# Kernel tuning notes

Hardware: AMD Instinct MI355X
Metric: run time of the kernel (lower is better)

The kernel has to match this reference:

```python
import jax, jax.numpy as jnp
import numpy as np

H = 64  # lstm_units
FORGET_BIAS = 1.0  # TF LSTMCell default


def setup_inputs() -> dict:
    key = jax.random.key(0)
    k1, k2, k3 = jax.random.split(key, 3)
    B, T = 256, 2048
    x = jax.random.normal(k1, (B, T, 1), dtype=jnp.float32)
    # Layer 1: LSTMCell(64), input dim 1 -> kernel [(1+64), 4*64]
    W1 = jax.random.normal(k2, (1 + H, 4 * H), dtype=jnp.float32) * 0.1
    b1 = jnp.zeros((4 * H,), dtype=jnp.float32)
    # Layer 2: LSTMCell(1), input dim 64 -> kernel [(64+1), 4*1]
    W2 = jax.random.normal(k3, (H + 1, 4), dtype=jnp.float32) * 0.1
    b2 = jnp.zeros((4,), dtype=jnp.float32)
    return {"x": x, "W1": W1, "b1": b1, "W2": W2, "b2": b2}


def _lstm_step(c, h, xt, W, b):
    # TF LSTMCell: gates from concat([x, h]) @ W + b, order i, j, f, o
    z = jnp.concatenate([xt, h], axis=-1) @ W + b
    i, j, f, o = jnp.split(z, 4, axis=-1)
    c_new = jax.nn.sigmoid(f + FORGET_BIAS) * c + jax.nn.sigmoid(i) * jnp.tanh(j)
    h_new = jax.nn.sigmoid(o) * jnpp_tanh(c_new) if False else jax.nn.sigmoid(o) * jnp.tanh(c_new)
    return c_new, h_new


def reference(x, W1, b1, W2, b2):
    # x: [B, T, 1] -> outputs of 2-layer stacked LSTM, final layer size 1
    B = x.shape[0]

    def step(carry, xt):
        c1, h1, c2, h2 = carry
        c1, h1 = _lstm_step(c1, h1, xt, W1, b1)
        c2, h2 = _lstm_step(c2, h2, h1, W2, b2)
        return (c1, h1, c2, h2), h2

    init = (
        jnp.zeros((B, H), x.dtype),
        jnp.zeros((B, H), x.dtype),
        jnp.zeros((B, 1), x.dtype),
        jnp.zeros((B, 1), x.dtype),
    )
    x_tbf = jnp.swapaxes(x, 0, 1)  # [T, B, 1]
    _, ys = jax.lax.scan(step, init, x_tbf)  # ys: [T, B, 1]
    return jnp.swapaxes(ys, 0, 1)  # [B, T, 1]
```

## Files before the change

kernel.cpp:

```cpp
#include <hip/hip_runtime.h>

constexpr int kT = 2048;
constexpr int kB = 256;
constexpr int kH = 64;

typedef __attribute__((ext_vector_type(2))) float f32x2;
typedef __attribute__((ext_vector_type(4))) float f32x4;

__device__ __forceinline__ float fast_sig(float x) {
    return __builtin_amdgcn_rcpf(1.0f + __expf(-x));
}
__device__ __forceinline__ float fast_tanh(float x) {
    float t = __expf(2.0f * x);
    return 1.0f - 2.0f * __builtin_amdgcn_rcpf(t + 1.0f);
}

__global__ __launch_bounds__(256)
__attribute__((amdgpu_waves_per_eu(1, 1)))
void lstm2_kernel(
    const float* __restrict__ x, const float* __restrict__ W1,
    const float* __restrict__ b1, const float* __restrict__ W2,
    const float* __restrict__ b2, float* __restrict__ out)
{
    __shared__ f32x4 x4_lds[kT / 4];
    __shared__ f32x4 out4_lds[kT / 4];
    __shared__ float h_lds[2][kH];
    __shared__ f32x4 z4_lds[2];

    float* x_lds = (float*)x4_lds;
    float* out_lds = (float*)out4_lds;

    const int tid = threadIdx.x;
    const int b = blockIdx.x;
    const int w = tid >> 6;
    const int l = tid & 63;
    const int g = l >> 4;
    const int s = l & 15;
    const int u = 16 * w + s;
    const int col = g * 64 + u;

    const f32x4* xg4 = (const f32x4*)(x + (size_t)b * kT);
    f32x4* outg4 = (f32x4*)(out + (size_t)b * kT);

    for (int i = tid; i < kT / 4; i += 256) x4_lds[i] = xg4[i];
    if (tid < kH) { h_lds[0][tid] = 0.0f; h_lds[1][tid] = 0.0f; }

    const float w0  = W1[col];
    const float b1g = b1[col];
    f32x2 wh[32];
    #pragma unroll
    for (int j = 0; j < 32; ++j) {
        wh[j].x = W1[(2 * j + 1) * 256 + col];
        wh[j].y = W1[(2 * j + 2) * 256 + col];
    }
    const float w2p0 = W2[(s +  0) * 4 + g];
    const float w2p1 = W2[(s + 16) * 4 + g];
    const float w2p2 = W2[(s + 32) * 4 + g];
    const float w2p3 = W2[(s + 48) * 4 + g];
    const float b2g  = b2[g];
    f32x4 w2t = ((const f32x4*)W2)[kH];

    #pragma unroll
    for (int j = 0; j < 32; ++j) asm volatile("" : "+v"(wh[j]));
    asm volatile("" : "+v"(w2t));

    float c1 = 0.0f, c2 = 0.0f, h2 = 0.0f;

    __syncthreads();

    #pragma unroll 1
    for (int t = 0; t < kT; ++t) {
        const int cur = t & 1, nxt = cur ^ 1;
        const float xt = x_lds[t];

        if (w == 0) {
            if (t >= 2) {
                const f32x4 z4 = z4_lds[nxt];
                const float zi = z4.x + h2 * w2t.x;
                const float zj = z4.y + h2 * w2t.y;
                const float zf = z4.z + h2 * w2t.z;
                const float zo = z4.w + h2 * w2t.w;
                c2 = fast_sig(zf + 1.0f) * c2 + fast_sig(zi) * fast_tanh(zj);
                h2 = fast_sig(zo) * fast_tanh(c2);
                if (l == 0) out_lds[t - 2] = h2;
            }
        } else if (w == 3) {
            if (t >= 1) {
                const float* hb = h_lds[cur];
                float pr = hb[s] * w2p0;
                pr = fmaf(hb[s + 16], w2p1, pr);
                pr = fmaf(hb[s + 32], w2p2, pr);
                pr = fmaf(hb[s + 48], w2p3, pr);
                pr += __shfl_xor(pr, 1);
                pr += __shfl_xor(pr, 2);
                pr += __shfl_xor(pr, 4);
                pr += __shfl_xor(pr, 8);
                if (s == 0) ((float*)&z4_lds[cur])[g] = pr + b2g;
            }
        }

        const f32x4* hb4 = (const f32x4*)h_lds[cur];
        f32x2 a0 = {fmaf(xt, w0, b1g), 0.0f};
        f32x2 a1 = {0.0f, 0.0f}, a2 = {0.0f, 0.0f}, a3 = {0.0f, 0.0f};
        #pragma unroll
        for (int k = 0; k < 16; k += 2) {
            const f32x4 hA = hb4[k];
            const f32x4 hB = hb4[k + 1];
            a0 += hA.xy * wh[2 * k];
            a1 += hA.zw * wh[2 * k + 1];
            a2 += hB.xy * wh[2 * k + 2];
            a3 += hB.zw * wh[2 * k + 3];
        }
        const f32x2 bb = (a0 + a1) + (a2 + a3);
        const float z = bb.x + bb.y;
        const float zz = (g == 1) ? 2.0f * z : ((g == 2) ? z + 1.0f : z);
        const float sg = fast_sig(zz);
        const float a = (g == 1) ? fmaf(2.0f, sg, -1.0f) : sg;
        const float ai = __shfl(a, s);
        const float aj = __shfl(a, s + 16);
        const float af = __shfl(a, s + 32);
        const float ao = __shfl(a, s + 48);
        c1 = fmaf(af, c1, ai * aj);
        const float h1n = ao * fast_tanh(c1);
        if (g == 0) h_lds[nxt][u] = h1n;

        __syncthreads();
    }

    if (w == 0) {
        {
            const f32x4 z4 = z4_lds[1];
            const float zi = z4.x + h2 * w2t.x;
            const float zj = z4.y + h2 * w2t.y;
            const float zf = z4.z + h2 * w2t.z;
            const float zo = z4.w + h2 * w2t.w;
            c2 = fast_sig(zf + 1.0f) * c2 + fast_sig(zi) * fast_tanh(zj);
            h2 = fast_sig(zo) * fast_tanh(c2);
            if (l == 0) out_lds[kT - 2] = h2;
        }
        {
            const float* hb = h_lds[0];
            float pr = hb[s] * w2p0;
            pr = fmaf(hb[s + 16], w2p1, pr);
            pr = fmaf(hb[s + 32], w2p2, pr);
            pr = fmaf(hb[s + 48], w2p3, pr);
            pr += __shfl_xor(pr, 1);
            pr += __shfl_xor(pr, 2);
            pr += __shfl_xor(pr, 4);
            pr += __shfl_xor(pr, 8);
            const float prb = pr + b2g;
            const float zi = __shfl(prb,  0) + h2 * w2t.x;
            const float zj = __shfl(prb, 16) + h2 * w2t.y;
            const float zf = __shfl(prb, 32) + h2 * w2t.z;
            const float zo = __shfl(prb, 48) + h2 * w2t.w;
            c2 = fast_sig(zf + 1.0f) * c2 + fast_sig(zi) * fast_tanh(zj);
            h2 = fast_sig(zo) * fast_tanh(c2);
            if (l == 0) out_lds[kT - 1] = h2;
        }
    }

    __syncthreads();
    for (int i = tid; i < kT / 4; i += 256) outg4[i] = out4_lds[i];
}

extern "C" void kernel_launch(void* const* d_in, const int* in_sizes, int n_in,
                              void* d_out, int out_size, void* d_ws, size_t ws_size,
                              hipStream_t stream) {
    const float* x  = (const float*)d_in[0];
    const float* W1 = (const float*)d_in[1];
    const float* b1 = (const float*)d_in[2];
    const float* W2 = (const float*)d_in[3];
    const float* b2 = (const float*)d_in[4];
    float* out = (float*)d_out;
    lstm2_kernel<<<kB, 256, 0, stream>>>(x, W1, b1, W2, b2, out);
}
```

Baseline: 1.276 ms.

## Decouple layer-2 recurrence into post-pass and use DPP for gate exchange

Each wave now computes one layer-2 input gate projection per step with a DPP wave reduction and stores it to a full-length LDS buffer. The scalar layer-2 recurrence then runs as a separate serial loop over all timesteps after the layer-1 loop. Gate columns are interleaved per lane so i/j/f/o exchange uses DPP quad permutes instead of cross-lane shuffles. This shortens the per-step critical path of the main loop but adds a serial tail of kT scalar LSTM steps and uses 32KB more LDS.

```diff
diff --git a/kernel.cpp b/kernel.cpp
--- a/kernel.cpp
+++ b/kernel.cpp
@@ -14,6 +14,26 @@
     float t = __expf(2.0f * x);
     return 1.0f - 2.0f * __builtin_amdgcn_rcpf(t + 1.0f);
 }
+template <int CTRL>
+__device__ __forceinline__ float dpp_mov(float v) {
+    return __int_as_float(__builtin_amdgcn_update_dpp(
+        0, __float_as_int(v), CTRL, 0xF, 0xF, true));
+}
+template <int CTRL>
+__device__ __forceinline__ float dpp_add(float acc) {
+    int t = __builtin_amdgcn_update_dpp(
+        0, __float_as_int(acc), CTRL, 0xF, 0xF, true);
+    return acc + __int_as_float(t);
+}
+__device__ __forceinline__ float wave_sum_to63(float v) {
+    v = dpp_add<0x111>(v);
+    v = dpp_add<0x112>(v);
+    v = dpp_add<0x114>(v);
+    v = dpp_add<0x118>(v);
+    v = dpp_add<0x142>(v);
+    v = dpp_add<0x143>(v);
+    return v;
+}
 
 __global__ __launch_bounds__(256)
 __attribute__((amdgpu_waves_per_eu(1, 1)))
@@ -24,19 +44,19 @@
 {
     __shared__ f32x4 x4_lds[kT / 4];
     __shared__ f32x4 out4_lds[kT / 4];
+    __shared__ f32x4 z4_lds[kT];
     __shared__ float h_lds[2][kH];
-    __shared__ f32x4 z4_lds[2];
 
     float* x_lds = (float*)x4_lds;
     float* out_lds = (float*)out4_lds;
+    float* z_lds = (float*)z4_lds;
 
     const int tid = threadIdx.x;
     const int b = blockIdx.x;
     const int w = tid >> 6;
     const int l = tid & 63;
-    const int g = l >> 4;
-    const int s = l & 15;
-    const int u = 16 * w + s;
+    const int g = l & 3;
+    const int u = 16 * w + (l >> 2);
     const int col = g * 64 + u;
 
     const f32x4* xg4 = (const f32x4*)(x + (size_t)b * kT);
@@ -53,52 +73,29 @@
         wh[j].x = W1[(2 * j + 1) * 256 + col];
         wh[j].y = W1[(2 * j + 2) * 256 + col];
     }
-    const float w2p0 = W2[(s +  0) * 4 + g];
-    const float w2p1 = W2[(s + 16) * 4 + g];
-    const float w2p2 = W2[(s + 32) * 4 + g];
-    const float w2p3 = W2[(s + 48) * 4 + g];
-    const float b2g  = b2[g];
-    f32x4 w2t = ((const f32x4*)W2)[kH];
+    const float w2c = W2[l * 4 + w];
+    const float b2w = b2[w];
 
     #pragma unroll
     for (int j = 0; j < 32; ++j) asm volatile("" : "+v"(wh[j]));
-    asm volatile("" : "+v"(w2t));
 
-    float c1 = 0.0f, c2 = 0.0f, h2 = 0.0f;
+    float c1 = 0.0f;
 
     __syncthreads();
 
     #pragma unroll 1
     for (int t = 0; t < kT; ++t) {
         const int cur = t & 1, nxt = cur ^ 1;
-        const float xt = x_lds[t];
 
-        if (w == 0) {
-            if (t >= 2) {
-                const f32x4 z4 = z4_lds[nxt];
-                const float zi = z4.x + h2 * w2t.x;
-                const float zj = z4.y + h2 * w2t.y;
-                const float zf = z4.z + h2 * w2t.z;
-                const float zo = z4.w + h2 * w2t.w;
-                c2 = fast_sig(zf + 1.0f) * c2 + fast_sig(zi) * fast_tanh(zj);
-                h2 = fast_sig(zo) * fast_tanh(c2);
-                if (l == 0) out_lds[t - 2] = h2;
-            }
-        } else if (w == 3) {
-            if (t >= 1) {
-                const float* hb = h_lds[cur];
-                float pr = hb[s] * w2p0;
-                pr = fmaf(hb[s + 16], w2p1, pr);
-                pr = fmaf(hb[s + 32], w2p2, pr);
-                pr = fmaf(hb[s + 48], w2p3, pr);
-                pr += __shfl_xor(pr, 1);
-                pr += __shfl_xor(pr, 2);
-                pr += __shfl_xor(pr, 4);
-                pr += __shfl_xor(pr, 8);
-                if (s == 0) ((float*)&z4_lds[cur])[g] = pr + b2g;
-            }
+        if (t >= 1) {
+            float pr = h_lds[cur][l] * w2c;
+            pr = wave_sum_to63(pr);
+            const float zt = __int_as_float(
+                __builtin_amdgcn_readlane(__float_as_int(pr), 63)) + b2w;
+            if (l == 0) z_lds[(t - 1) * 4 + w] = zt;
         }
 
+        const float xt = x_lds[t];
         const f32x4* hb4 = (const f32x4*)h_lds[cur];
         f32x2 a0 = {fmaf(xt, w0, b1g), 0.0f};
         f32x2 a1 = {0.0f, 0.0f}, a2 = {0.0f, 0.0f}, a3 = {0.0f, 0.0f};
@@ -116,50 +113,42 @@
         const float zz = (g == 1) ? 2.0f * z : ((g == 2) ? z + 1.0f : z);
         const float sg = fast_sig(zz);
         const float a = (g == 1) ? fmaf(2.0f, sg, -1.0f) : sg;
-        const float ai = __shfl(a, s);
-        const float aj = __shfl(a, s + 16);
-        const float af = __shfl(a, s + 32);
-        const float ao = __shfl(a, s + 48);
-        c1 = fmaf(af, c1, ai * aj);
+        const float aj = dpp_mov<0xB1>(a);
+        const float af = dpp_mov<0x4E>(a);
+        const float ao = dpp_mov<0x1B>(a);
+        c1 = fmaf(af, c1, a * aj);
         const float h1n = ao * fast_tanh(c1);
         if (g == 0) h_lds[nxt][u] = h1n;
 
         __syncthreads();
     }
 
+    {
+        float pr = h_lds[0][l] * w2c;
+        pr = wave_sum_to63(pr);
+        const float zt = __int_as_float(
+            __builtin_amdgcn_readlane(__float_as_int(pr), 63)) + b2w;
+        if (l == 0) z_lds[(kT - 1) * 4 + w] = zt;
+    }
+    __syncthreads();
+
     if (w == 0) {
-        {
-            const f32x4 z4 = z4_lds[1];
+        const f32x4 w2t = ((const f32x4*)W2)[kH];
+        float c2 = 0.0f, h2 = 0.0f;
+        #pragma unroll 2
+        for (int t2 = 0; t2 < kT; ++t2) {
+            const f32x4 z4 = z4_lds[t2];
             const float zi = z4.x + h2 * w2t.x;
             const float zj = z4.y + h2 * w2t.y;
             const float zf = z4.z + h2 * w2t.z;
             const float zo = z4.w + h2 * w2t.w;
             c2 = fast_sig(zf + 1.0f) * c2 + fast_sig(zi) * fast_tanh(zj);
             h2 = fast_sig(zo) * fast_tanh(c2);
-            if (l == 0) out_lds[kT - 2] = h2;
-        }
-        {
-            const float* hb = h_lds[0];
-            float pr = hb[s] * w2p0;
-            pr = fmaf(hb[s + 16], w2p1, pr);
-            pr = fmaf(hb[s + 32], w2p2, pr);
-            pr = fmaf(hb[s + 48], w2p3, pr);
-            pr += __shfl_xor(pr, 1);
-            pr += __shfl_xor(pr, 2);
-            pr += __shfl_xor(pr, 4);
-            pr += __shfl_xor(pr, 8);
-            const float prb = pr + b2g;
-            const float zi = __shfl(prb,  0) + h2 * w2t.x;
-            const float zj = __shfl(prb, 16) + h2 * w2t.y;
-            const float zf = __shfl(prb, 32) + h2 * w2t.z;
-            const float zo = __shfl(prb, 48) + h2 * w2t.w;
-            c2 = fast_sig(zf + 1.0f) * c2 + fast_sig(zi) * fast_tanh(zj);
-            h2 = fast_sig(zo) * fast_tanh(c2);
-            if (l == 0) out_lds[kT - 1] = h2;
+            if (l == 0) out_lds[t2] = h2;
         }
     }
+    __syncthreads();
 
-    __syncthreads();
     for (int i = tid; i < kT / 4; i += 256) outg4[i] = out4_lds[i];
 }
 
```

After: 1.219 ms. 4.5% less time.
